# Optimization experiments

Hardware: AMD Instinct MI355X
Metric: run time of the kernel (lower is better)

## Reference

```python
import jax, jax.numpy as jnp
import numpy as np

N = 100000   # neurons
R = 4        # receptor types (tau_syns has 4 entries)
E = 2000000  # synapses
T = 50       # timesteps
B = 1        # batch
DT = 1.0
DAMP = 0.3      # dampening_factor for pseudo-derivative
REC_DAMP = 0.5  # recurrent_dampening_factor


@jax.custom_vjp
def spike_function(v_scaled, dampening_factor):
    return (v_scaled > 0.0).astype(v_scaled.dtype)


def _spike_fwd(v_scaled, dampening_factor):
    return spike_function(v_scaled, dampening_factor), (v_scaled, dampening_factor)


def _spike_bwd(res, g):
    v_scaled, d = res
    dz_dv = d * jnp.maximum(1.0 - jnp.abs(v_scaled), 0.0)  # pseudo_derivative
    return (g * dz_dv, jnp.zeros_like(d))


spike_function.defvjp(_spike_fwd, _spike_bwd)


def setup_inputs() -> dict:
    key = jax.random.key(0)
    ks = jax.random.split(key, 11)
    tau_syns = jnp.array([5.5, 8.5, 2.8, 5.8], jnp.float32)
    return {
        "w_rec": jax.random.normal(ks[0], (E,), jnp.float32) * 0.01,
        "x_ext": jax.random.normal(ks[1], (T, B, N * R), jnp.float32) * 0.05,
        "v0": jax.random.uniform(ks[2], (B, N), jnp.float32),
        "v_th": jnp.ones((N,), jnp.float32),           # normalized threshold
        "v_reset": jnp.zeros((N,), jnp.float32),       # normalized reset
        "t_ref": jnp.full((N,), 2.0, jnp.float32),
        "decay": jax.random.uniform(ks[3], (N,), jnp.float32, minval=0.8, maxval=0.99),
        "current_factor": jax.random.uniform(ks[4], (N,), jnp.float32, minval=0.5, maxval=1.5),
        "e_l_current": jax.random.normal(ks[5], (N,), jnp.float32) * 0.01,
        "asc_amps": jax.random.normal(ks[6], (N, 2), jnp.float32) * 0.01,
        "asc_decay": jax.random.uniform(ks[7], (N, 2), jnp.float32, minval=0.7, maxval=0.99),
        "syn_decay": jnp.exp(-DT / tau_syns),
        "psc_init": jnp.float32(np.e) / tau_syns,
        "pre_idx": jax.random.randint(ks[8], (E,), 0, N, jnp.int32),
        "post_idx": jax.random.randint(ks[9], (E,), 0, N, jnp.int32),
        "receptor_idx": jax.random.randint(ks[10], (E,), 0, R, jnp.int32),
    }


def reference(w_rec, x_ext, v0, v_th, v_reset, t_ref, decay, current_factor,
              e_l_current, asc_amps, asc_decay, syn_decay, psc_init,
              pre_idx, post_idx, receptor_idx):
    # flat (neuron, receptor) slot layout: slot = neuron*R + receptor
    seg_ids = post_idx * R + receptor_idx
    syn_d = jnp.tile(syn_decay, N)[None, :]   # [1, N*R]
    psc_i = jnp.tile(psc_init, N)[None, :]    # [1, N*R]
    damp = jnp.float32(DAMP)

    def step(carry, x_t):
        z, v, r, asc, psc, psc_rise = carry
        # gradient dampening on recurrent spikes (same forward value as z)
        rec_z = REC_DAMP * z + (1.0 - REC_DAMP) * jax.lax.stop_gradient(z)
        # sparse gather-multiply-scatter: [B,E] -> [B, N*R]
        contrib = rec_z[:, pre_idx] * w_rec[None, :]
        rec_in = jax.vmap(
            lambda c: jax.ops.segment_sum(c, seg_ids, num_segments=N * R)
        )(contrib)
        inputs = rec_in + x_t
        # double-exponential synaptic filtering
        new_psc_rise = psc_rise * syn_d + inputs * psc_i
        new_psc = psc * syn_d + DT * syn_d * psc_rise
        # after-spike currents (2 channels)
        new_asc = asc_decay[None] * asc + z[..., None] * asc_amps[None]
        input_current = new_psc.reshape(B, N, R).sum(-1) + asc.sum(-1)  # [B,N]
        # soft reset from previous spike
        reset_current = z * (v_reset - v_th)[None]
        new_v = decay[None] * v + current_factor[None] * (input_current + e_l_current[None]) + reset_current
        # normalized voltage (E_L normalized to 0, so normalizer = v_th)
        v_sc = (new_v - v_th[None]) / v_th[None]
        new_z = spike_function(v_sc, damp)
        new_z = jnp.where(r > 0.0, jnp.zeros_like(new_z), new_z)  # refractory
        new_r = jnp.maximum(r - DT + new_z * t_ref[None], 0.0)
        return (new_z, new_v, new_r, new_asc, new_psc, new_psc_rise), new_z

    carry0 = (
        jnp.zeros((B, N), jnp.float32),      # z
        v0,                                  # v
        jnp.zeros((B, N), jnp.float32),      # refractory counter
        jnp.zeros((B, N, 2), jnp.float32),   # asc
        jnp.zeros((B, N * R), jnp.float32),  # psc
        jnp.zeros((B, N * R), jnp.float32),  # psc_rise
    )
    _, spikes = jax.lax.scan(step, carry0, x_ext)
    return spikes  # [T, B, N]
```

## Files before the change

### kernel.cpp

```cpp
#include <hip/hip_runtime.h>


constexpr int RR  = 4;
constexpr int BS  = 1024;
constexpr int BKN = 512;
constexpr int NCH = 512;

__global__ void count_kernel(const int* __restrict__ post, int* __restrict__ ghist,
                             unsigned long long* __restrict__ mA,
                             unsigned long long* __restrict__ mB,
                             unsigned* __restrict__ barr,
                             int E, int CH, int NBK, int nmask, int nbar) {
    __shared__ int h[256];
    for (int i = threadIdx.x; i < NBK; i += blockDim.x) h[i] = 0;
    __syncthreads();
    const int b = blockIdx.x, lo = b * CH, hi = min(lo + CH, E);
    for (int e = lo + threadIdx.x; e < hi; e += blockDim.x)
        atomicAdd(&h[post[e] >> 9], 1);
    __syncthreads();
    for (int i = threadIdx.x; i < NBK; i += blockDim.x)
        ghist[i * NCH + b] = h[i];
    int g = blockIdx.x * blockDim.x + threadIdx.x;
    int gs = gridDim.x * blockDim.x;
    for (int i = g; i < nmask; i += gs) { mA[i] = 0ull; mB[i] = 0ull; }
    for (int i = g; i < nbar; i += gs) barr[i] = 0u;
}

__global__ void scanA_kernel(int* __restrict__ ghist, int* __restrict__ rtot,
                             int* __restrict__ ptot) {
    __shared__ int s[NCH];
    const int i = blockIdx.x, tid = threadIdx.x;
    int v = ghist[i * NCH + tid];
    s[tid] = v;
    __syncthreads();
    for (int off = 1; off < NCH; off <<= 1) {
        int t = (tid >= off) ? s[tid - off] : 0;
        __syncthreads();
        s[tid] += t;
        __syncthreads();
    }
    ghist[i * NCH + tid] = s[tid] - v;
    if (tid == NCH - 1) {
        int tot = s[tid];
        rtot[i] = tot;
        ptot[i] = (tot + 3) & ~3;
    }
}

__global__ void scanB_kernel(const int* __restrict__ rtot, const int* __restrict__ ptot,
                             int* __restrict__ bstart,
                             unsigned* __restrict__ epack, float* __restrict__ ew,
                             int NBK) {
    __shared__ int s[256];
    const int tid = threadIdx.x;
    int v = (tid < NBK) ? ptot[tid] : 0;
    s[tid] = v;
    __syncthreads();
    for (int off = 1; off < 256; off <<= 1) {
        int t = (tid >= off) ? s[tid - off] : 0;
        __syncthreads();
        s[tid] += t;
        __syncthreads();
    }
    if (tid < NBK) bstart[tid] = s[tid] - v;
    if (tid == NBK - 1) bstart[NBK] = s[tid];
    __syncthreads();
    if (tid < NBK) {
        int base = bstart[tid];
        for (int k = base + rtot[tid]; k < base + ptot[tid]; ++k) {
            epack[k] = 0u; ew[k] = 0.f;
        }
    }
}

__global__ void fill_kernel(const int* __restrict__ pre, const int* __restrict__ post,
                            const int* __restrict__ rc, const float* __restrict__ w,
                            const int* __restrict__ ghist, const int* __restrict__ bstart,
                            unsigned* __restrict__ epack, float* __restrict__ ew,
                            int E, int CH, int NBK) {
    __shared__ int cur[256];
    const int b = blockIdx.x;
    for (int i = threadIdx.x; i < NBK; i += blockDim.x)
        cur[i] = bstart[i] + ghist[i * NCH + b];
    __syncthreads();
    const int lo = b * CH, hi = min(lo + CH, E);
    for (int e = lo + threadIdx.x; e < hi; e += blockDim.x) {
        int pn = post[e];
        int k = atomicAdd(&cur[pn >> 9], 1);
        epack[k] = (unsigned)pre[e] | ((unsigned)rc[e] << 18)
                 | ((unsigned)(pn & (BKN - 1)) << 20);
        ew[k] = w[e];
    }
}

__device__ __forceinline__ void test4(const uint4 pk, const float4 wv,
                                      const unsigned long long* smask,
                                      float* sacc) {
    unsigned a = pk.x & 0x3FFFFu, b = pk.y & 0x3FFFFu;
    unsigned c = pk.z & 0x3FFFFu, d = pk.w & 0x3FFFFu;
    if ((smask[a >> 6] >> (a & 63)) & 1ull) atomicAdd(&sacc[pk.x >> 18], wv.x);
    if ((smask[b >> 6] >> (b & 63)) & 1ull) atomicAdd(&sacc[pk.y >> 18], wv.y);
    if ((smask[c >> 6] >> (c & 63)) & 1ull) atomicAdd(&sacc[pk.z >> 18], wv.z);
    if ((smask[d >> 6] >> (d & 63)) & 1ull) atomicAdd(&sacc[pk.w >> 18], wv.w);
}

__global__ void __launch_bounds__(BS, 4)
sim_kernel(const float4* __restrict__ x_ext4,
           const float* __restrict__ v0,  const float* __restrict__ v_th,
           const float* __restrict__ v_rst, const float* __restrict__ t_rf,
           const float* __restrict__ decay, const float* __restrict__ curf,
           const float* __restrict__ e_l,
           const float2* __restrict__ aamps, const float2* __restrict__ adec,
           const float* __restrict__ syn_d4, const float* __restrict__ psc_i4,
           const uint4* __restrict__ epack4, const float4* __restrict__ ew4,
           const int* __restrict__ bstart,
           unsigned long long* __restrict__ mA, unsigned long long* __restrict__ mB,
           unsigned* __restrict__ barr,
           float* __restrict__ out, int N, int nmask, int T)
{
    extern __shared__ unsigned long long sdyn[];
    unsigned long long* smask = sdyn;
    float* sacc = (float*)(sdyn + nmask);
    const int tid = threadIdx.x;
    const int n = blockIdx.x * BKN + tid;
    const bool own = (tid < BKN) && (n < N);
    const unsigned nblk = gridDim.x;

    float psc0 = 0.f, psc1 = 0.f, psc2 = 0.f, psc3 = 0.f;
    float pr0 = 0.f, pr1 = 0.f, pr2 = 0.f, pr3 = 0.f;
    float vv = 0.f, rr_ = 0.f, zz = 0.f, a0 = 0.f, a1 = 0.f;
    float vth = 1.f, dvr = 0.f, trf = 0.f, dec = 0.f, cf = 0.f, el = 0.f;
    float aa0 = 0.f, aa1 = 0.f, ad0 = 0.f, ad1 = 0.f;
    if (own) {
        vv  = v0[n];
        vth = v_th[n];  dvr = v_rst[n] - vth;
        trf = t_rf[n];  dec = decay[n];
        cf  = curf[n];  el  = e_l[n];
        float2 aa = aamps[n]; aa0 = aa.x; aa1 = aa.y;
        float2 ad = adec[n];  ad0 = ad.x; ad1 = ad.y;
    }
    const float sd0 = syn_d4[0], sd1 = syn_d4[1], sd2 = syn_d4[2], sd3 = syn_d4[3];
    const float pi0 = psc_i4[0], pi1 = psc_i4[1], pi2 = psc_i4[2], pi3 = psc_i4[3];

    const int q_lo = bstart[blockIdx.x] >> 2;
    const int q_hi = bstart[blockIdx.x + 1] >> 2;
    const int i0 = q_lo + tid, i1 = i0 + BS, i2 = i1 + BS, i3 = i2 + BS;
    const uint4 z4 = make_uint4(0u, 0u, 0u, 0u);
    const float4 zf = make_float4(0.f, 0.f, 0.f, 0.f);
    uint4  qa = (i0 < q_hi) ? epack4[i0] : z4;
    uint4  qb = (i1 < q_hi) ? epack4[i1] : z4;
    uint4  qc = (i2 < q_hi) ? epack4[i2] : z4;
    uint4  qd = (i3 < q_hi) ? epack4[i3] : z4;
    float4 wa = (i0 < q_hi) ? ew4[i0] : zf;
    float4 wb = (i1 < q_hi) ? ew4[i1] : zf;
    float4 wc = (i2 < q_hi) ? ew4[i2] : zf;
    float4 wd = (i3 < q_hi) ? ew4[i3] : zf;
    const bool overflow = (q_hi - q_lo) > 4 * BS;

    const int g = blockIdx.x & 7;
    const unsigned gsize = (nblk - (unsigned)g + 7u) >> 3;

    float4 xt = own ? x_ext4[n] : zf;

    for (int t = 0; t < T; ++t) {
        unsigned long long m0 = 0ull, m1 = 0ull;
        if (t > 0) {
            const unsigned long long* gm = ((t - 1) & 1) ? mB : mA;
            if (tid < nmask)
                m0 = __hip_atomic_load(&gm[tid], __ATOMIC_RELAXED,
                                       __HIP_MEMORY_SCOPE_AGENT);
            if (tid + BS < nmask)
                m1 = __hip_atomic_load(&gm[tid + BS], __ATOMIC_RELAXED,
                                       __HIP_MEMORY_SCOPE_AGENT);
        }
        sacc[tid] = 0.f; sacc[tid + BS] = 0.f;
        if (tid < nmask) smask[tid] = m0;
        if (tid + BS < nmask) smask[tid + BS] = m1;
        int anyspk = __syncthreads_or((m0 | m1) != 0ull ? 1 : 0);

        if (anyspk) {
            test4(qa, wa, smask, sacc);
            test4(qb, wb, smask, sacc);
            test4(qc, wc, smask, sacc);
            test4(qd, wd, smask, sacc);
            if (overflow) {
                for (int q = q_lo + tid + 4 * BS; q < q_hi; q += BS)
                    test4(epack4[q], ew4[q], smask, sacc);
            }
        }
        __syncthreads();

        float nz = 0.f;
        if (own) {
            float acc0 = sacc[tid * 4 + 0], acc1 = sacc[tid * 4 + 1];
            float acc2 = sacc[tid * 4 + 2], acc3 = sacc[tid * 4 + 3];
            float i0_ = acc0 + xt.x, i1_ = acc1 + xt.y;
            float i2_ = acc2 + xt.z, i3_ = acc3 + xt.w;
            float npr0 = pr0 * sd0 + i0_ * pi0;
            float npr1 = pr1 * sd1 + i1_ * pi1;
            float npr2 = pr2 * sd2 + i2_ * pi2;
            float npr3 = pr3 * sd3 + i3_ * pi3;
            float npc0 = psc0 * sd0 + sd0 * pr0;
            float npc1 = psc1 * sd1 + sd1 * pr1;
            float npc2 = psc2 * sd2 + sd2 * pr2;
            float npc3 = psc3 * sd3 + sd3 * pr3;
            float in_cur = npc0 + npc1 + npc2 + npc3;
            psc0 = npc0; psc1 = npc1; psc2 = npc2; psc3 = npc3;
            pr0 = npr0; pr1 = npr1; pr2 = npr2; pr3 = npr3;

            float asum = a0 + a1;
            a0 = ad0 * a0 + zz * aa0;
            a1 = ad1 * a1 + zz * aa1;

            float nv = dec * vv + cf * (in_cur + asum + el) + zz * dvr;
            nz = (nv > vth) ? 1.f : 0.f;
            if (rr_ > 0.f) nz = 0.f;
            rr_ = fmaxf(rr_ - 1.f + nz * trf, 0.f);
            vv = nv; zz = nz;
        }

        unsigned long long bal = __ballot(nz > 0.f);
        unsigned long long* gmo = (t & 1) ? mB : mA;
        if (own && (tid & 63) == 0)
            __hip_atomic_store(&gmo[n >> 6], bal, __ATOMIC_RELAXED,
                               __HIP_MEMORY_SCOPE_AGENT);

        if (t + 1 < T) {
            asm volatile("s_waitcnt vmcnt(0)" ::: "memory");
            if (own) out[(size_t)t * N + n] = nz;
            float4 xtn = own ? x_ext4[(size_t)(t + 1) * N + n] : zf;
            __syncthreads();
            if (tid == 0) {
                unsigned* bg  = barr + (size_t)t * 160 + (size_t)g * 16;
                unsigned* btp = barr + (size_t)t * 160 + 128;
                unsigned* rl  = barr + (size_t)t * 160 + 144;
                bool done = false;
                unsigned old = __hip_atomic_fetch_add(bg, 1u, __ATOMIC_RELAXED,
                                                      __HIP_MEMORY_SCOPE_AGENT);
                if (old == gsize - 1u) {
                    unsigned ot = __hip_atomic_fetch_add(btp, 1u, __ATOMIC_RELAXED,
                                                         __HIP_MEMORY_SCOPE_AGENT);
                    if (ot == 7u) {
                        __hip_atomic_store(rl, 1u, __ATOMIC_RELAXED,
                                           __HIP_MEMORY_SCOPE_AGENT);
                        done = true;
                    }
                }
                if (!done)
                    while (!__hip_atomic_load(rl, __ATOMIC_RELAXED,
                                              __HIP_MEMORY_SCOPE_AGENT))
                        __builtin_amdgcn_s_sleep(1);
            }
            __syncthreads();
            xt = xtn;
        } else {
            if (own) out[(size_t)t * N + n] = nz;
        }
    }
}

extern "C" void kernel_launch(void* const* d_in, const int* in_sizes, int n_in,
                              void* d_out, int out_size, void* d_ws, size_t ws_size,
                              hipStream_t stream) {
    const float* w_rec = (const float*)d_in[0];
    const float* x_ext = (const float*)d_in[1];
    const float* v0    = (const float*)d_in[2];
    const float* v_th  = (const float*)d_in[3];
    const float* v_rst = (const float*)d_in[4];
    const float* t_rf  = (const float*)d_in[5];
    const float* decay = (const float*)d_in[6];
    const float* curf  = (const float*)d_in[7];
    const float* e_l   = (const float*)d_in[8];
    const float* aamps = (const float*)d_in[9];
    const float* adec  = (const float*)d_in[10];
    const float* syn_d = (const float*)d_in[11];
    const float* psc_i = (const float*)d_in[12];
    const int*   pre   = (const int*)d_in[13];
    const int*   post  = (const int*)d_in[14];
    const int*   rc    = (const int*)d_in[15];

    const int E = in_sizes[0];
    const int N = in_sizes[2];
    const int T = in_sizes[1] / (N * RR);
    const int nmask = (N + 63) / 64;
    const int NBK = (N + BKN - 1) / BKN;
    const int CH  = (E + NCH - 1) / NCH;
    const int nbar = 160 * T;
    const int EP  = E + 4 * NBK;

    char* ws = (char*)d_ws;
    unsigned* epack  = (unsigned*)ws;                     ws += (size_t)EP * 4;
    float*    ew     = (float*)ws;                        ws += (size_t)EP * 4;
    unsigned long long* maskA = (unsigned long long*)ws;  ws += (size_t)nmask * 8;
    unsigned long long* maskB = (unsigned long long*)ws;  ws += (size_t)nmask * 8;
    int* ghist       = (int*)ws;                          ws += (size_t)NBK * NCH * 4;
    int* rtot        = (int*)ws;                          ws += (size_t)NBK * 4;
    int* ptot        = (int*)ws;                          ws += (size_t)NBK * 4;
    int* bstart      = (int*)ws;                          ws += (size_t)(NBK + 1) * 4;
    unsigned* barr   = (unsigned*)ws;

    count_kernel<<<NCH, 256, 0, stream>>>(post, ghist, maskA, maskB, barr,
                                          E, CH, NBK, nmask, nbar);
    scanA_kernel<<<NBK, NCH, 0, stream>>>(ghist, rtot, ptot);
    scanB_kernel<<<1, 256, 0, stream>>>(rtot, ptot, bstart, epack, ew, NBK);
    fill_kernel<<<NCH, 256, 0, stream>>>(pre, post, rc, w_rec, ghist, bstart,
                                         epack, ew, E, CH, NBK);

    const size_t smbytes = (size_t)nmask * 8 + (size_t)BKN * RR * 4;
    sim_kernel<<<NBK, BS, smbytes, stream>>>(
        (const float4*)x_ext, v0, v_th, v_rst, t_rf, decay, curf, e_l,
        (const float2*)aamps, (const float2*)adec, syn_d, psc_i,
        (const uint4*)epack, (const float4*)ew, bstart, maskA, maskB, barr,
        (float*)d_out, N, nmask, T);
}
```

Measured before the change: 504.0 us.

## Split grid barrier into arrive/wait to overlap synaptic scatter with barrier latency

Reorders each timestep so the spike (z) is computed first from the previous psc_rise, then published and the grid barrier is arrived at. Next, the synaptic accumulation for the previous step's spikes runs, and only then does the block wait on the barrier and load the new spike masks. The scatter work now overlaps the barrier latency instead of sitting after it. This relies on the algebraic fact that new_psc depends only on the old psc_rise. It adds register pressure and reorders the state updates, so correctness depends on that dependency split being exact.

Measured after the change: 483.1 us. -4.2%, faster.

```diff
diff --git a/kernel.cpp b/kernel.cpp
--- a/kernel.cpp
+++ b/kernel.cpp
@@ -160,23 +160,60 @@
     const int g = blockIdx.x & 7;
     const unsigned gsize = (nblk - (unsigned)g + 7u) >> 3;
 
+    for (int i = tid; i < nmask; i += BS) smask[i] = 0ull;
+    sacc[tid] = 0.f; sacc[tid + BS] = 0.f;
     float4 xt = own ? x_ext4[n] : zf;
+    int anyspk = 0;
+    __syncthreads();
 
     for (int t = 0; t < T; ++t) {
-        unsigned long long m0 = 0ull, m1 = 0ull;
-        if (t > 0) {
-            const unsigned long long* gm = ((t - 1) & 1) ? mB : mA;
-            if (tid < nmask)
-                m0 = __hip_atomic_load(&gm[tid], __ATOMIC_RELAXED,
+        float nz = 0.f;
+        float npc0, npc1, npc2, npc3;
+        if (own) {
+            npc0 = psc0 * sd0 + sd0 * pr0;
+            npc1 = psc1 * sd1 + sd1 * pr1;
+            npc2 = psc2 * sd2 + sd2 * pr2;
+            npc3 = psc3 * sd3 + sd3 * pr3;
+            float in_cur = npc0 + npc1 + npc2 + npc3;
+            float asum = a0 + a1;
+            float nv = dec * vv + cf * (in_cur + asum + el) + zz * dvr;
+            nz = (nv > vth) ? 1.f : 0.f;
+            if (rr_ > 0.f) nz = 0.f;
+            rr_ = fmaxf(rr_ - 1.f + nz * trf, 0.f);
+            a0 = ad0 * a0 + zz * aa0;
+            a1 = ad1 * a1 + zz * aa1;
+            psc0 = npc0; psc1 = npc1; psc2 = npc2; psc3 = npc3;
+            vv = nv;
+        }
+        const bool lastT = (t + 1 >= T);
+
+        unsigned long long bal = __ballot(nz > 0.f);
+        if (!lastT) {
+            unsigned long long* gmo = (t & 1) ? mB : mA;
+            if (own && (tid & 63) == 0)
+                __hip_atomic_store(&gmo[n >> 6], bal, __ATOMIC_RELAXED,
+                                   __HIP_MEMORY_SCOPE_AGENT);
+            asm volatile("s_waitcnt vmcnt(0)" ::: "memory");
+        }
+        __syncthreads();
+
+        bool i_released = false;
+        if (!lastT && tid == 0) {
+            unsigned* bg  = barr + (size_t)t * 160 + (size_t)g * 16;
+            unsigned* btp = barr + (size_t)t * 160 + 128;
+            unsigned* rl  = barr + (size_t)t * 160 + 144;
+            unsigned old = __hip_atomic_fetch_add(bg, 1u, __ATOMIC_RELAXED,
+                                                  __HIP_MEMORY_SCOPE_AGENT);
+            if (old == gsize - 1u) {
+                unsigned ot = __hip_atomic_fetch_add(btp, 1u, __ATOMIC_RELAXED,
+                                                     __HIP_MEMORY_SCOPE_AGENT);
+                if (ot == 7u) {
+                    __hip_atomic_store(rl, 1u, __ATOMIC_RELAXED,
                                        __HIP_MEMORY_SCOPE_AGENT);
-            if (tid + BS < nmask)
-                m1 = __hip_atomic_load(&gm[tid + BS], __ATOMIC_RELAXED,
-                                       __HIP_MEMORY_SCOPE_AGENT);
-        }
-        sacc[tid] = 0.f; sacc[tid + BS] = 0.f;
-        if (tid < nmask) smask[tid] = m0;
-        if (tid + BS < nmask) smask[tid + BS] = m1;
-        int anyspk = __syncthreads_or((m0 | m1) != 0ull ? 1 : 0);
+                    i_released = true;
+                }
+            }
+        }
 
         if (anyspk) {
             test4(qa, wa, smask, sacc);
@@ -190,71 +227,42 @@
         }
         __syncthreads();
 
-        float nz = 0.f;
         if (own) {
             float acc0 = sacc[tid * 4 + 0], acc1 = sacc[tid * 4 + 1];
             float acc2 = sacc[tid * 4 + 2], acc3 = sacc[tid * 4 + 3];
-            float i0_ = acc0 + xt.x, i1_ = acc1 + xt.y;
-            float i2_ = acc2 + xt.z, i3_ = acc3 + xt.w;
-            float npr0 = pr0 * sd0 + i0_ * pi0;
-            float npr1 = pr1 * sd1 + i1_ * pi1;
-            float npr2 = pr2 * sd2 + i2_ * pi2;
-            float npr3 = pr3 * sd3 + i3_ * pi3;
-            float npc0 = psc0 * sd0 + sd0 * pr0;
-            float npc1 = psc1 * sd1 + sd1 * pr1;
-            float npc2 = psc2 * sd2 + sd2 * pr2;
-            float npc3 = psc3 * sd3 + sd3 * pr3;
-            float in_cur = npc0 + npc1 + npc2 + npc3;
-            psc0 = npc0; psc1 = npc1; psc2 = npc2; psc3 = npc3;
-            pr0 = npr0; pr1 = npr1; pr2 = npr2; pr3 = npr3;
-
-            float asum = a0 + a1;
-            a0 = ad0 * a0 + zz * aa0;
-            a1 = ad1 * a1 + zz * aa1;
-
-            float nv = dec * vv + cf * (in_cur + asum + el) + zz * dvr;
-            nz = (nv > vth) ? 1.f : 0.f;
-            if (rr_ > 0.f) nz = 0.f;
-            rr_ = fmaxf(rr_ - 1.f + nz * trf, 0.f);
-            vv = nv; zz = nz;
-        }
-
-        unsigned long long bal = __ballot(nz > 0.f);
-        unsigned long long* gmo = (t & 1) ? mB : mA;
-        if (own && (tid & 63) == 0)
-            __hip_atomic_store(&gmo[n >> 6], bal, __ATOMIC_RELAXED,
-                               __HIP_MEMORY_SCOPE_AGENT);
-
-        if (t + 1 < T) {
-            asm volatile("s_waitcnt vmcnt(0)" ::: "memory");
-            if (own) out[(size_t)t * N + n] = nz;
+            sacc[tid * 4 + 0] = 0.f; sacc[tid * 4 + 1] = 0.f;
+            sacc[tid * 4 + 2] = 0.f; sacc[tid * 4 + 3] = 0.f;
+            pr0 = pr0 * sd0 + (acc0 + xt.x) * pi0;
+            pr1 = pr1 * sd1 + (acc1 + xt.y) * pi1;
+            pr2 = pr2 * sd2 + (acc2 + xt.z) * pi2;
+            pr3 = pr3 * sd3 + (acc3 + xt.w) * pi3;
+            out[(size_t)t * N + n] = nz;
+            zz = nz;
+        }
+
+        if (!lastT) {
             float4 xtn = own ? x_ext4[(size_t)(t + 1) * N + n] : zf;
-            __syncthreads();
-            if (tid == 0) {
-                unsigned* bg  = barr + (size_t)t * 160 + (size_t)g * 16;
-                unsigned* btp = barr + (size_t)t * 160 + 128;
-                unsigned* rl  = barr + (size_t)t * 160 + 144;
-                bool done = false;
-                unsigned old = __hip_atomic_fetch_add(bg, 1u, __ATOMIC_RELAXED,
-                                                      __HIP_MEMORY_SCOPE_AGENT);
-                if (old == gsize - 1u) {
-                    unsigned ot = __hip_atomic_fetch_add(btp, 1u, __ATOMIC_RELAXED,
-                                                         __HIP_MEMORY_SCOPE_AGENT);
-                    if (ot == 7u) {
-                        __hip_atomic_store(rl, 1u, __ATOMIC_RELAXED,
-                                           __HIP_MEMORY_SCOPE_AGENT);
-                        done = true;
-                    }
-                }
-                if (!done)
-                    while (!__hip_atomic_load(rl, __ATOMIC_RELAXED,
-                                              __HIP_MEMORY_SCOPE_AGENT))
-                        __builtin_amdgcn_s_sleep(1);
+
+            if (tid == 0 && !i_released) {
+                unsigned* rl = barr + (size_t)t * 160 + 144;
+                while (!__hip_atomic_load(rl, __ATOMIC_RELAXED,
+                                          __HIP_MEMORY_SCOPE_AGENT))
+                    __builtin_amdgcn_s_sleep(1);
             }
             __syncthreads();
+
+            const unsigned long long* gm = (t & 1) ? mB : mA;
+            unsigned long long m0 = 0ull, m1 = 0ull;
+            if (tid < nmask)
+                m0 = __hip_atomic_load(&gm[tid], __ATOMIC_RELAXED,
+                                       __HIP_MEMORY_SCOPE_AGENT);
+            if (tid + BS < nmask)
+                m1 = __hip_atomic_load(&gm[tid + BS], __ATOMIC_RELAXED,
+                                       __HIP_MEMORY_SCOPE_AGENT);
+            if (tid < nmask) smask[tid] = m0;
+            if (tid + BS < nmask) smask[tid + BS] = m1;
+            anyspk = __syncthreads_or((m0 | m1) != 0ull ? 1 : 0);
             xt = xtn;
-        } else {
-            if (own) out[(size_t)t * N + n] = nz;
         }
     }
 }
```
